# Optimization experiments

Measured on AMD Instinct MI355X. Metric: run time of the kernel, lower is better.

## Reference

```python
import math
import jax, jax.numpy as jnp
import numpy as np

B, DIM, H = 16, 1024, 16
HD = DIM // H                      # 64
P_ORIG = 1024                      # num_patches arg
NP = math.ceil(math.sqrt(P_ORIG)) ** 2 // 2   # 512 attended tokens
ALPHA, BETA, GAMMA = 1.9, 3.8, 15.2           # iRPE euc config, ratio=1.9
NUM_BUCKETS = 2 * int(BETA) + 1               # 7


def _rp_bucket(L):
    """Static euclidean-distance relative-position buckets (iRPE 'euc')."""
    E = int(math.ceil(math.sqrt(L)))
    flat = np.arange(E * E)
    pos = np.stack([flat // E, flat % E], axis=1)[:L].astype(np.float64)  # [L,2]
    diff = pos[:, None, :] - pos[None, :, :]
    dis = np.round(np.sqrt((diff ** 2).sum(-1)))
    far = np.round(ALPHA + np.log(np.maximum(dis, 1e-9) / ALPHA)
                   / math.log(GAMMA / ALPHA) * (BETA - ALPHA))
    idx = np.where(dis <= ALPHA, np.round(dis), np.minimum(far, BETA)).astype(np.int32)
    idx = idx - idx.min()
    return jnp.asarray(idx)  # [L,L] int32 in [0, int(BETA)]

RP_BUCKET = _rp_bucket(NP)


def setup_inputs() -> dict:
    key = jax.random.key(0)
    ks = jax.random.split(key, 7)
    s = 0.02
    return {
        "x": jax.random.normal(ks[0], (B, P_ORIG, DIM), dtype=jnp.float32),
        "wq": jax.random.normal(ks[1], (DIM, DIM), dtype=jnp.float32) * s,
        "wk": jax.random.normal(ks[2], (DIM, DIM), dtype=jnp.float32) * s,
        "wv": jax.random.normal(ks[3], (DIM, DIM), dtype=jnp.float32) * s,
        "rpe_w": jax.random.normal(ks[4], (HD, NUM_BUCKETS), dtype=jnp.float32) * s,
        "proj_w": jax.random.normal(ks[5], (DIM, DIM), dtype=jnp.float32) * s,
        "proj_b": jax.random.normal(ks[6], (DIM,), dtype=jnp.float32) * s,
    }


def reference(x, wq, wk, wv, rpe_w, proj_w, proj_b):
    # F.pad on token axis with pad = NP - N (negative => crop)
    pad = NP - x.shape[1]
    if pad >= 0:
        x = jnp.pad(x, ((0, 0), (0, pad), (0, 0)))
    else:
        x = x[:, :NP, :]
    b = x.shape[0]
    scale = HD ** (-0.5)

    def heads(t):  # [b,NP,DIM] -> [b,H,NP,HD]
        return t.reshape(b, NP, H, HD).transpose(0, 2, 1, 3)

    q = heads(x @ wq.T)
    k = heads(x @ wk.T)
    v = heads(x @ wv.T)

    attn = jnp.einsum('bhid,bhjd->bhij', q, k) * scale
    # contextual RPE on keys (transposed): bias[b,h,i,j] = q[b,h,i,:] . W[:, bucket[i,j]]
    lt = jnp.einsum('bhid,dn->bhin', q, rpe_w)                 # [b,H,NP,NB]
    bias = jnp.take_along_axis(lt, RP_BUCKET[None, None, :, :], axis=3)  # [b,H,NP,NP]
    attn = jax.nn.softmax(attn + bias, axis=-1)

    out = jnp.einsum('bhij,bhjd->bhid', attn, v)
    out = out.transpose(0, 2, 1, 3).reshape(b, NP, DIM)
    out = out @ proj_w.T + proj_b
    return out[:, :P_ORIG, :]
```

## Files before the change

kernel.cpp:

```cpp
#include <hip/hip_runtime.h>

typedef __attribute__((ext_vector_type(8))) __bf16 bf16x8;
typedef __attribute__((ext_vector_type(4))) float f32x4;

#define DEVI static __device__ __forceinline__

DEVI unsigned short f2bf(float f) {
  unsigned int u = __float_as_uint(f);
  u += 0x7fffu + ((u >> 16) & 1u);
  return (unsigned short)(u >> 16);
}
DEVI float bf2f(unsigned short s) {
  return __uint_as_float(((unsigned int)s) << 16);
}

union Frag {
  bf16x8 v;
  unsigned short h[8];
  unsigned int w[4];
};

typedef __attribute__((address_space(1))) const void gv_t;
typedef __attribute__((address_space(3))) void sv_t;
#define GLOAD_LDS16(g, l) __builtin_amdgcn_global_load_lds((gv_t*)(g), (sv_t*)(l), 16, 0, 0)

__global__ __launch_bounds__(256) void k_convert(
    const float* __restrict__ x, const float* __restrict__ wq,
    const float* __restrict__ wk, const float* __restrict__ wv,
    const float* __restrict__ pw,
    unsigned short* __restrict__ xb, unsigned short* __restrict__ wb)
{
  int t = blockIdx.x * 256 + threadIdx.x;
  const float* src;
  unsigned short* dst;
  if (t < 1048576) {
    long e0 = (long)t << 3;
    int m = (int)(e0 >> 10), cc = (int)(e0 & 1023);
    int b = m >> 9, i = m & 511;
    src = x + (((long)(b << 10) + i) << 10) + cc;
    dst = xb + ((long)m << 10) + cc;
  } else {
    long e0 = (long)(t - 1048576) << 3;
    int mat = (int)(e0 >> 20);
    long off = e0 & 1048575;
    const float* s = (mat == 0) ? wq : (mat == 1) ? wk : (mat == 2) ? wv : pw;
    src = s + off;
    dst = wb + e0;
  }
  float4 a = *(const float4*)src;
  float4 b4 = *(const float4*)(src + 4);
  uint4 o;
  o.x = f2bf(a.x)  | ((unsigned)f2bf(a.y)  << 16);
  o.y = f2bf(a.z)  | ((unsigned)f2bf(a.w)  << 16);
  o.z = f2bf(b4.x) | ((unsigned)f2bf(b4.y) << 16);
  o.w = f2bf(b4.z) | ((unsigned)f2bf(b4.w) << 16);
  *(uint4*)dst = o;
}

__global__ __launch_bounds__(256) void k_bucket(unsigned char* __restrict__ bkt)
{
  int t = blockIdx.x * 256 + threadIdx.x;
  int i = t >> 9, j = t & 511;
  int ir = i / 23, ic = i - ir * 23;
  int jr = j / 23, jc = j - jr * 23;
  int dy = ir - jr, dx = ic - jc;
  double dis = rint(sqrt((double)(dy * dy + dx * dx)));
  int v;
  if (dis <= 1.9) {
    v = (int)rint(dis);
  } else {
    double far = rint(1.9 + log(dis / 1.9) * (1.9 / log(8.0)));
    v = (int)fmin(far, 3.8);
  }
  bkt[t] = (unsigned char)v;
}

template<int MODE>
__global__ __launch_bounds__(256) void k_gemm(
    const unsigned short* __restrict__ A,
    const unsigned short* __restrict__ Bw,
    unsigned short* __restrict__ qh, unsigned short* __restrict__ kh,
    unsigned short* __restrict__ vt,
    float* __restrict__ out, const float* __restrict__ bias)
{
  __shared__ unsigned short sA[128 * 32];
  __shared__ unsigned short sB[128 * 32];
  const int tid = threadIdx.x;
  const int tileN = blockIdx.x, tileM = blockIdx.y;
  const int w = tid >> 6, lane = tid & 63;
  const int g = lane >> 4, c = lane & 15;
  const int wm = w >> 1, wn = w & 1;

  f32x4 acc[4][4] = {};

  const unsigned short* ga = A  + ((long)tileM * 128 + (tid >> 2)) * 1024 + (tid & 3) * 8;
  const unsigned short* gb = Bw + ((long)tileN * 128 + (tid >> 2)) * 1024 + (tid & 3) * 8;
  char* la = (char*)sA + tid * 16;
  char* lb = (char*)sB + tid * 16;

  for (int kt = 0; kt < 32; ++kt) {
    __syncthreads();
    const unsigned short* gak = ga + kt * 32;
    const unsigned short* gbk = gb + kt * 32;
    GLOAD_LDS16(gak,              la);
    GLOAD_LDS16(gak + 64 * 1024,  la + 4096);
    GLOAD_LDS16(gbk,              lb);
    GLOAD_LDS16(gbk + 64 * 1024,  lb + 4096);
    __syncthreads();

    bf16x8 af[4], bf[4];
#pragma unroll
    for (int mi = 0; mi < 4; ++mi)
      af[mi] = *(const bf16x8*)(sA + (wm * 64 + mi * 16 + c) * 32 + g * 8);
#pragma unroll
    for (int ni = 0; ni < 4; ++ni)
      bf[ni] = *(const bf16x8*)(sB + (wn * 64 + ni * 16 + c) * 32 + g * 8);
#pragma unroll
    for (int mi = 0; mi < 4; ++mi)
#pragma unroll
      for (int ni = 0; ni < 4; ++ni)
        acc[mi][ni] = __builtin_amdgcn_mfma_f32_16x16x32_bf16(af[mi], bf[ni], acc[mi][ni], 0, 0, 0);
  }

  const int m0 = tileM * 128 + wm * 64;
  const int n0 = tileN * 128 + wn * 64;

  if (MODE == 0) {
#pragma unroll
    for (int mi = 0; mi < 4; ++mi) {
      int mrow = m0 + mi * 16 + g * 4;
      int b = mrow >> 9, i = mrow & 511;
#pragma unroll
      for (int ni = 0; ni < 4; ++ni) {
        int n = n0 + ni * 16 + c;
        int mat = n >> 10;
        int cc = n & 1023;
        int h = cc >> 6, d = cc & 63;
        long bh = (long)(b * 16 + h);
        if (mat == 2) {
          unsigned int w0 = f2bf(acc[mi][ni][0]) | ((unsigned)f2bf(acc[mi][ni][1]) << 16);
          unsigned int w1 = f2bf(acc[mi][ni][2]) | ((unsigned)f2bf(acc[mi][ni][3]) << 16);
          *(uint2*)(vt + (bh * 64 + d) * 512 + i) = make_uint2(w0, w1);
        } else {
          unsigned short* dst = (mat == 0 ? qh : kh) + (bh * 512 + i) * 64 + d;
#pragma unroll
          for (int r = 0; r < 4; ++r)
            dst[(long)r * 64] = f2bf(acc[mi][ni][r]);
        }
      }
    }
  } else {
#pragma unroll
    for (int mi = 0; mi < 4; ++mi) {
      int mrow = m0 + mi * 16 + g * 4;
#pragma unroll
      for (int ni = 0; ni < 4; ++ni) {
        int n = n0 + ni * 16 + c;
        float bv = bias[n];
#pragma unroll
        for (int r = 0; r < 4; ++r)
          out[(long)(mrow + r) * 1024 + n] = acc[mi][ni][r] + bv;
      }
    }
  }
}

__global__ __launch_bounds__(512) void k_attn(
    const unsigned short* __restrict__ qh, const unsigned short* __restrict__ kh,
    const unsigned short* __restrict__ vt, const float* __restrict__ rpe,
    const unsigned char* __restrict__ bkt, unsigned short* __restrict__ ao)
{
  __shared__ float lt_lds[512 * 9];
  const int bh = blockIdx.x;
  const int b = bh >> 4, h = bh & 15;
  const int w = threadIdx.x >> 6, lane = threadIdx.x & 63;
  const int g = lane >> 4, c = lane & 15;
  const int qbase = w * 64;
  const unsigned short* Q = qh + (long)bh * 512 * 64;
  const unsigned short* K = kh + (long)bh * 512 * 64;
  const unsigned short* V = vt + (long)bh * 64 * 512;

  Frag qu[4][2];
#pragma unroll
  for (int it = 0; it < 4; ++it)
#pragma unroll
    for (int kk = 0; kk < 2; ++kk)
      qu[it][kk].v = *(const bf16x8*)(Q + (qbase + it * 16 + c) * 64 + kk * 32 + g * 8);

  float lt[4][7] = {};
#pragma unroll
  for (int kk = 0; kk < 2; ++kk)
#pragma unroll
    for (int tt = 0; tt < 8; ++tt) {
      int d = kk * 32 + g * 8 + tt;
      const float* rr = rpe + d * 7;
      float r0 = rr[0], r1 = rr[1], r2 = rr[2], r3 = rr[3], r4 = rr[4], r5 = rr[5], r6 = rr[6];
#pragma unroll
      for (int it = 0; it < 4; ++it) {
        float qv = bf2f(qu[it][kk].h[tt]);
        lt[it][0] += qv * r0; lt[it][1] += qv * r1; lt[it][2] += qv * r2;
        lt[it][3] += qv * r3; lt[it][4] += qv * r4; lt[it][5] += qv * r5;
        lt[it][6] += qv * r6;
      }
    }
#pragma unroll
  for (int it = 0; it < 4; ++it)
#pragma unroll
    for (int n = 0; n < 7; ++n) {
      float v = lt[it][n];
      v += __shfl_xor(v, 16);
      v += __shfl_xor(v, 32);
      if (g == 0) lt_lds[(qbase + it * 16 + c) * 9 + n] = v;
    }

  f32x4 oacc[4][4] = {};
  float mrun[4] = {-1e30f, -1e30f, -1e30f, -1e30f};
  float lp[4] = {0.f, 0.f, 0.f, 0.f};

  for (int jb = 0; jb < 512; jb += 32) {
    const int jp0 = jb + (c >> 2) * 8 + (c & 3);
    Frag kf[2][2];
#pragma unroll
    for (int jt = 0; jt < 2; ++jt)
#pragma unroll
      for (int kk = 0; kk < 2; ++kk)
        kf[jt][kk].v = *(const bf16x8*)(K + (jp0 + jt * 4) * 64 + kk * 32 + g * 8);

    f32x4 s[2][4];
#pragma unroll
    for (int jt = 0; jt < 2; ++jt)
#pragma unroll
      for (int it = 0; it < 4; ++it) {
        f32x4 z = {0.f, 0.f, 0.f, 0.f};
        z = __builtin_amdgcn_mfma_f32_16x16x32_bf16(kf[jt][0].v, qu[it][0].v, z, 0, 0, 0);
        s[jt][it] = __builtin_amdgcn_mfma_f32_16x16x32_bf16(kf[jt][1].v, qu[it][1].v, z, 0, 0, 0);
      }

    Frag pfr[4];
#pragma unroll
    for (int it = 0; it < 4; ++it) {
      int irow = qbase + it * 16 + c;
      float sv[8];
#pragma unroll
      for (int jt = 0; jt < 2; ++jt) {
        unsigned int bb = *(const unsigned int*)(bkt + (long)irow * 512 + jb + g * 8 + jt * 4);
#pragma unroll
        for (int r = 0; r < 4; ++r) {
          int bno = (bb >> (8 * r)) & 255;
          float bias = lt_lds[irow * 9 + bno];
          sv[jt * 4 + r] = s[jt][it][r] * 0.125f + bias;
        }
      }
      float pm = sv[0];
#pragma unroll
      for (int t = 1; t < 8; ++t) pm = fmaxf(pm, sv[t]);
      pm = fmaxf(pm, __shfl_xor(pm, 16));
      pm = fmaxf(pm, __shfl_xor(pm, 32));
      float mnew = fmaxf(mrun[it], pm);
      float fsc = __expf(mrun[it] - mnew);
      mrun[it] = mnew;
      lp[it] *= fsc;
#pragma unroll
      for (int dt = 0; dt < 4; ++dt) oacc[dt][it] = oacc[dt][it] * fsc;
      float psum = 0.f;
#pragma unroll
      for (int t = 0; t < 8; ++t) {
        float e = __expf(sv[t] - mnew);
        psum += e;
        pfr[it].h[t] = f2bf(e);
      }
      lp[it] += psum;
    }

    bf16x8 vf[4];
#pragma unroll
    for (int dt = 0; dt < 4; ++dt)
      vf[dt] = *(const bf16x8*)(V + (dt * 16 + c) * 512 + jb + g * 8);

#pragma unroll
    for (int dt = 0; dt < 4; ++dt)
#pragma unroll
      for (int it = 0; it < 4; ++it)
        oacc[dt][it] = __builtin_amdgcn_mfma_f32_16x16x32_bf16(vf[dt], pfr[it].v, oacc[dt][it], 0, 0, 0);
  }

  float li[4];
#pragma unroll
  for (int it = 0; it < 4; ++it) {
    float v = lp[it];
    v += __shfl_xor(v, 16);
    v += __shfl_xor(v, 32);
    li[it] = 1.0f / v;
  }
#pragma unroll
  for (int dt = 0; dt < 4; ++dt)
#pragma unroll
    for (int it = 0; it < 4; ++it) {
      int irow = qbase + it * 16 + c;
      int d0 = dt * 16 + g * 4;
      unsigned int w0 = f2bf(oacc[dt][it][0] * li[it]) | ((unsigned)f2bf(oacc[dt][it][1] * li[it]) << 16);
      unsigned int w1 = f2bf(oacc[dt][it][2] * li[it]) | ((unsigned)f2bf(oacc[dt][it][3] * li[it]) << 16);
      *(uint2*)(ao + ((long)(b * 512 + irow)) * 1024 + h * 64 + d0) = make_uint2(w0, w1);
    }
}

extern "C" void kernel_launch(void* const* d_in, const int* in_sizes, int n_in,
                              void* d_out, int out_size, void* d_ws, size_t ws_size,
                              hipStream_t stream) {
  const float* x   = (const float*)d_in[0];
  const float* wq  = (const float*)d_in[1];
  const float* wk  = (const float*)d_in[2];
  const float* wv  = (const float*)d_in[3];
  const float* rpe = (const float*)d_in[4];
  const float* pw  = (const float*)d_in[5];
  const float* pb  = (const float*)d_in[6];
  float* out = (float*)d_out;

  char* ws = (char*)d_ws;
  unsigned short* xb  = (unsigned short*)(ws);
  unsigned short* wb  = (unsigned short*)(ws + 16777216);
  unsigned short* qhp = (unsigned short*)(ws + 25165824);
  unsigned short* khp = (unsigned short*)(ws + 41943040);
  unsigned short* vtp = (unsigned short*)(ws + 58720256);
  unsigned char*  bkt = (unsigned char*)(ws + 75497472);
  unsigned short* aop = xb;

  k_convert<<<dim3(6144), dim3(256), 0, stream>>>(x, wq, wk, wv, pw, xb, wb);
  k_bucket<<<dim3(1024), dim3(256), 0, stream>>>(bkt);
  k_gemm<0><<<dim3(24, 64), dim3(256), 0, stream>>>(xb, wb, qhp, khp, vtp, nullptr, nullptr);
  k_attn<<<dim3(256), dim3(512), 0, stream>>>(qhp, khp, vtp, rpe, bkt, aop);
  k_gemm<1><<<dim3(8, 64), dim3(256), 0, stream>>>(aop, wb + 3 * 1048576, nullptr, nullptr, nullptr, out, pb);
}
```

Before: 165.3 us.

## Triple-buffer GEMM with 256x128 tiles, XCD swizzle, split attention over query segments

The GEMM kernel now uses 512 threads computing 256x128 tiles. It triple-buffers its direct-to-LDS global loads with manual waitcnt and barriers, uses an XOR-swizzled LDS layout to avoid bank conflicts, remaps block IDs across XCDs, and raises MFMA priority with setprio. The attention kernel is split into four query segments per head with 256-thread blocks, giving 1024 blocks instead of 256 to fill the GPU better, at the cost of re-reading K/V per segment. The changes aim at load latency stalls, LDS conflicts and low occupancy in the attention stage.

```diff
diff --git a/kernel.cpp b/kernel.cpp
--- a/kernel.cpp
+++ b/kernel.cpp
@@ -22,7 +22,7 @@
 
 typedef __attribute__((address_space(1))) const void gv_t;
 typedef __attribute__((address_space(3))) void sv_t;
-#define GLOAD_LDS16(g, l) __builtin_amdgcn_global_load_lds((gv_t*)(g), (sv_t*)(l), 16, 0, 0)
+#define GLOAD_LDS16(gp, lp) __builtin_amdgcn_global_load_lds((gv_t*)(gp), (sv_t*)(lp), 16, 0, 0)
 
 __global__ __launch_bounds__(256) void k_convert(
     const float* __restrict__ x, const float* __restrict__ wq,
@@ -76,53 +76,83 @@
 }
 
 template<int MODE>
-__global__ __launch_bounds__(256) void k_gemm(
+__global__ __launch_bounds__(512) void k_gemm(
     const unsigned short* __restrict__ A,
     const unsigned short* __restrict__ Bw,
     unsigned short* __restrict__ qh, unsigned short* __restrict__ kh,
     unsigned short* __restrict__ vt,
     float* __restrict__ out, const float* __restrict__ bias)
 {
-  __shared__ unsigned short sA[128 * 32];
-  __shared__ unsigned short sB[128 * 32];
+  __shared__ unsigned short sL[3 * 12288];
+
+  const int NTN = (MODE == 0) ? 24 : 8;
+  const int nwg = (MODE == 0) ? 768 : 256;
+  const int cpx = nwg / 8;
+  const int bid = blockIdx.x;
+  const int swz = (bid & 7) * cpx + (bid >> 3);
+  const int tileN = swz % NTN, tileM = swz / NTN;
+
   const int tid = threadIdx.x;
-  const int tileN = blockIdx.x, tileM = blockIdx.y;
   const int w = tid >> 6, lane = tid & 63;
   const int g = lane >> 4, c = lane & 15;
   const int wm = w >> 1, wn = w & 1;
 
+  const int sk = (g * 8) ^ ((c & 8) ? 16 : 0);
+  int offA[4], offB[4];
+#pragma unroll
+  for (int i = 0; i < 4; ++i) {
+    offA[i] = (wm * 4 + i) * 512 + c * 32 + sk;
+    offB[i] = 8192 + (wn * 4 + i) * 512 + c * 32 + sk;
+  }
+
+  const int colb = ((lane & 3) * 8) ^ ((lane >= 32) ? 16 : 0);
+  const unsigned short* gA0 = A  + ((long)(tileM * 256 + w * 32 + (lane >> 2))) * 1024 + colb;
+  const unsigned short* gA1 = gA0 + 16 * 1024;
+  const unsigned short* gB0 = Bw + ((long)(tileN * 128 + w * 16 + (lane >> 2))) * 1024 + colb;
+
+#define STAGE(ktile, buf) do {                                             \
+    const long ko_ = (long)(ktile) * 32;                                   \
+    char* base_ = (char*)sL + (buf) * 24576;                               \
+    GLOAD_LDS16(gA0 + ko_, base_ + (w * 2) * 1024 + lane * 16);            \
+    GLOAD_LDS16(gA1 + ko_, base_ + (w * 2 + 1) * 1024 + lane * 16);        \
+    GLOAD_LDS16(gB0 + ko_, base_ + 16384 + w * 1024 + lane * 16);          \
+  } while (0)
+
   f32x4 acc[4][4] = {};
 
-  const unsigned short* ga = A  + ((long)tileM * 128 + (tid >> 2)) * 1024 + (tid & 3) * 8;
-  const unsigned short* gb = Bw + ((long)tileN * 128 + (tid >> 2)) * 1024 + (tid & 3) * 8;
-  char* la = (char*)sA + tid * 16;
-  char* lb = (char*)sB + tid * 16;
-
-  for (int kt = 0; kt < 32; ++kt) {
-    __syncthreads();
-    const unsigned short* gak = ga + kt * 32;
-    const unsigned short* gbk = gb + kt * 32;
-    GLOAD_LDS16(gak,              la);
-    GLOAD_LDS16(gak + 64 * 1024,  la + 4096);
-    GLOAD_LDS16(gbk,              lb);
-    GLOAD_LDS16(gbk + 64 * 1024,  lb + 4096);
-    __syncthreads();
-
+  STAGE(0, 0);
+  STAGE(1, 1);
+
+  int rb = 0, wbuf = 2;
+  for (int t = 0; t < 32; ++t) {
+    asm volatile("s_waitcnt vmcnt(3)" ::: "memory");
+    __builtin_amdgcn_s_barrier();
+    int kt = t + 2; if (kt > 31) kt = 31;
+    STAGE(kt, wbuf);
+
+    const unsigned short* lb = sL + rb * 12288;
     bf16x8 af[4], bf[4];
 #pragma unroll
-    for (int mi = 0; mi < 4; ++mi)
-      af[mi] = *(const bf16x8*)(sA + (wm * 64 + mi * 16 + c) * 32 + g * 8);
-#pragma unroll
-    for (int ni = 0; ni < 4; ++ni)
-      bf[ni] = *(const bf16x8*)(sB + (wn * 64 + ni * 16 + c) * 32 + g * 8);
+    for (int i = 0; i < 4; ++i) af[i] = *(const bf16x8*)(lb + offA[i]);
+#pragma unroll
+    for (int i = 0; i < 4; ++i) bf[i] = *(const bf16x8*)(lb + offB[i]);
+
+    __builtin_amdgcn_s_setprio(1);
 #pragma unroll
     for (int mi = 0; mi < 4; ++mi)
 #pragma unroll
       for (int ni = 0; ni < 4; ++ni)
         acc[mi][ni] = __builtin_amdgcn_mfma_f32_16x16x32_bf16(af[mi], bf[ni], acc[mi][ni], 0, 0, 0);
-  }
-
-  const int m0 = tileM * 128 + wm * 64;
+    __builtin_amdgcn_s_setprio(0);
+    asm volatile("s_waitcnt lgkmcnt(0)" ::: "memory");
+
+    rb = (rb == 2) ? 0 : rb + 1;
+    wbuf = (wbuf == 2) ? 0 : wbuf + 1;
+  }
+  asm volatile("s_waitcnt vmcnt(0)" ::: "memory");
+#undef STAGE
+
+  const int m0 = tileM * 256 + wm * 64;
   const int n0 = tileN * 128 + wn * 64;
 
   if (MODE == 0) {
@@ -165,29 +195,32 @@
   }
 }
 
-__global__ __launch_bounds__(512) void k_attn(
+__global__ __launch_bounds__(256) void k_attn(
     const unsigned short* __restrict__ qh, const unsigned short* __restrict__ kh,
     const unsigned short* __restrict__ vt, const float* __restrict__ rpe,
     const unsigned char* __restrict__ bkt, unsigned short* __restrict__ ao)
 {
-  __shared__ float lt_lds[512 * 9];
-  const int bh = blockIdx.x;
-  const int b = bh >> 4, h = bh & 15;
+  __shared__ float lt_lds[128 * 9];
+  const int bid = blockIdx.x;
+  const int sbid = (bid & 7) * 128 + (bid >> 3);
+  const int head = sbid >> 2, seg = sbid & 3;
+  const int b = head >> 4, h = head & 15;
   const int w = threadIdx.x >> 6, lane = threadIdx.x & 63;
   const int g = lane >> 4, c = lane & 15;
-  const int qbase = w * 64;
-  const unsigned short* Q = qh + (long)bh * 512 * 64;
-  const unsigned short* K = kh + (long)bh * 512 * 64;
-  const unsigned short* V = vt + (long)bh * 64 * 512;
-
-  Frag qu[4][2];
-#pragma unroll
-  for (int it = 0; it < 4; ++it)
+  const int qloc = w * 32;
+  const int qg = seg * 128 + qloc;
+  const unsigned short* Q = qh + (long)head * 512 * 64;
+  const unsigned short* K = kh + (long)head * 512 * 64;
+  const unsigned short* V = vt + (long)head * 64 * 512;
+
+  Frag qu[2][2];
+#pragma unroll
+  for (int it = 0; it < 2; ++it)
 #pragma unroll
     for (int kk = 0; kk < 2; ++kk)
-      qu[it][kk].v = *(const bf16x8*)(Q + (qbase + it * 16 + c) * 64 + kk * 32 + g * 8);
-
-  float lt[4][7] = {};
+      qu[it][kk].v = *(const bf16x8*)(Q + (qg + it * 16 + c) * 64 + kk * 32 + g * 8);
+
+  float lt[2][7] = {};
 #pragma unroll
   for (int kk = 0; kk < 2; ++kk)
 #pragma unroll
@@ -196,7 +229,7 @@
       const float* rr = rpe + d * 7;
       float r0 = rr[0], r1 = rr[1], r2 = rr[2], r3 = rr[3], r4 = rr[4], r5 = rr[5], r6 = rr[6];
 #pragma unroll
-      for (int it = 0; it < 4; ++it) {
+      for (int it = 0; it < 2; ++it) {
         float qv = bf2f(qu[it][kk].h[tt]);
         lt[it][0] += qv * r0; lt[it][1] += qv * r1; lt[it][2] += qv * r2;
         lt[it][3] += qv * r3; lt[it][4] += qv * r4; lt[it][5] += qv * r5;
@@ -204,18 +237,18 @@
       }
     }
 #pragma unroll
-  for (int it = 0; it < 4; ++it)
+  for (int it = 0; it < 2; ++it)
 #pragma unroll
     for (int n = 0; n < 7; ++n) {
       float v = lt[it][n];
       v += __shfl_xor(v, 16);
       v += __shfl_xor(v, 32);
-      if (g == 0) lt_lds[(qbase + it * 16 + c) * 9 + n] = v;
-    }
-
-  f32x4 oacc[4][4] = {};
-  float mrun[4] = {-1e30f, -1e30f, -1e30f, -1e30f};
-  float lp[4] = {0.f, 0.f, 0.f, 0.f};
+      if (g == 0) lt_lds[(qloc + it * 16 + c) * 9 + n] = v;
+    }
+
+  f32x4 oacc[4][2] = {};
+  float mrun[2] = {-1e30f, -1e30f};
+  float lp[2] = {0.f, 0.f};
 
   for (int jb = 0; jb < 512; jb += 32) {
     const int jp0 = jb + (c >> 2) * 8 + (c & 3);
@@ -226,28 +259,29 @@
       for (int kk = 0; kk < 2; ++kk)
         kf[jt][kk].v = *(const bf16x8*)(K + (jp0 + jt * 4) * 64 + kk * 32 + g * 8);
 
-    f32x4 s[2][4];
+    f32x4 s[2][2];
 #pragma unroll
     for (int jt = 0; jt < 2; ++jt)
 #pragma unroll
-      for (int it = 0; it < 4; ++it) {
+      for (int it = 0; it < 2; ++it) {
         f32x4 z = {0.f, 0.f, 0.f, 0.f};
         z = __builtin_amdgcn_mfma_f32_16x16x32_bf16(kf[jt][0].v, qu[it][0].v, z, 0, 0, 0);
         s[jt][it] = __builtin_amdgcn_mfma_f32_16x16x32_bf16(kf[jt][1].v, qu[it][1].v, z, 0, 0, 0);
       }
 
-    Frag pfr[4];
-#pragma unroll
-    for (int it = 0; it < 4; ++it) {
-      int irow = qbase + it * 16 + c;
+    Frag pfr[2];
+#pragma unroll
+    for (int it = 0; it < 2; ++it) {
+      int lrow = qloc + it * 16 + c;
+      int grow = qg + it * 16 + c;
       float sv[8];
 #pragma unroll
       for (int jt = 0; jt < 2; ++jt) {
-        unsigned int bb = *(const unsigned int*)(bkt + (long)irow * 512 + jb + g * 8 + jt * 4);
+        unsigned int bb = *(const unsigned int*)(bkt + (long)grow * 512 + jb + g * 8 + jt * 4);
 #pragma unroll
         for (int r = 0; r < 4; ++r) {
           int bno = (bb >> (8 * r)) & 255;
-          float bias = lt_lds[irow * 9 + bno];
+          float bias = lt_lds[lrow * 9 + bno];
           sv[jt * 4 + r] = s[jt][it][r] * 0.125f + bias;
         }
       }
@@ -280,13 +314,13 @@
 #pragma unroll
     for (int dt = 0; dt < 4; ++dt)
 #pragma unroll
-      for (int it = 0; it < 4; ++it)
+      for (int it = 0; it < 2; ++it)
         oacc[dt][it] = __builtin_amdgcn_mfma_f32_16x16x32_bf16(vf[dt], pfr[it].v, oacc[dt][it], 0, 0, 0);
   }
 
-  float li[4];
-#pragma unroll
-  for (int it = 0; it < 4; ++it) {
+  float li[2];
+#pragma unroll
+  for (int it = 0; it < 2; ++it) {
     float v = lp[it];
     v += __shfl_xor(v, 16);
     v += __shfl_xor(v, 32);
@@ -295,8 +329,8 @@
 #pragma unroll
   for (int dt = 0; dt < 4; ++dt)
 #pragma unroll
-    for (int it = 0; it < 4; ++it) {
-      int irow = qbase + it * 16 + c;
+    for (int it = 0; it < 2; ++it) {
+      int irow = qg + it * 16 + c;
       int d0 = dt * 16 + g * 4;
       unsigned int w0 = f2bf(oacc[dt][it][0] * li[it]) | ((unsigned)f2bf(oacc[dt][it][1] * li[it]) << 16);
       unsigned int w1 = f2bf(oacc[dt][it][2] * li[it]) | ((unsigned)f2bf(oacc[dt][it][3] * li[it]) << 16);
@@ -327,7 +361,7 @@
 
   k_convert<<<dim3(6144), dim3(256), 0, stream>>>(x, wq, wk, wv, pw, xb, wb);
   k_bucket<<<dim3(1024), dim3(256), 0, stream>>>(bkt);
-  k_gemm<0><<<dim3(24, 64), dim3(256), 0, stream>>>(xb, wb, qhp, khp, vtp, nullptr, nullptr);
-  k_attn<<<dim3(256), dim3(512), 0, stream>>>(qhp, khp, vtp, rpe, bkt, aop);
-  k_gemm<1><<<dim3(8, 64), dim3(256), 0, stream>>>(aop, wb + 3 * 1048576, nullptr, nullptr, nullptr, out, pb);
-}
+  k_gemm<0><<<dim3(768), dim3(512), 0, stream>>>(xb, wb, qhp, khp, vtp, nullptr, nullptr);
+  k_attn<<<dim3(1024), dim3(256), 0, stream>>>(qhp, khp, vtp, rpe, bkt, aop);
+  k_gemm<1><<<dim3(256), dim3(512), 0, stream>>>(aop, wb + 3 * 1048576, nullptr, nullptr, nullptr, out, pb);
+}
```

Result: slower. 177.3 us (+7.2%).
